# Kernel optimization log

Hardware: AMD Instinct MI355X
Metric: run time of the kernel (lower is better)

The kernel has to match this reference:

```python
import jax, jax.numpy as jnp
import numpy as np

B, V = 256, 128000
NOISE_MIN = 1e-10


def setup_inputs() -> dict:
    key = jax.random.key(0)
    k_log, k_temp, k_noise = jax.random.split(key, 3)
    logits = jax.random.normal(k_log, (B, V), dtype=jnp.float32)
    temperatures = jax.random.uniform(k_temp, (B,), dtype=jnp.float32)
    # first quarter of rows use greedy decoding (temperature <= 0)
    temperatures = temperatures.at[: B // 4].set(0.0)
    # torch's empty_like().exponential_(1) -> Exp(1) noise, passed explicitly for determinism
    noise = jax.random.exponential(k_noise, (B, V), dtype=jnp.float32)
    return {"logits": logits, "temperatures": temperatures, "noise": noise}


def reference(logits, temperatures, noise):
    logits = logits.astype(jnp.float32)  # [B, V]
    greedy = temperatures <= 0           # [B]
    # avoid div-by-zero on greedy rows; their result is overwritten by jnp.where below
    safe_t = jnp.where(greedy, 1.0, temperatures)
    probs = jax.nn.softmax(logits / safe_t[:, None], axis=-1)          # [B, V]
    sampled_tok = jnp.argmax(probs / jnp.maximum(noise, NOISE_MIN), axis=-1)  # Gumbel-style sampling
    greedy_tok = jnp.argmax(logits, axis=-1)
    return jnp.where(greedy, greedy_tok, sampled_tok).astype(jnp.int64)
```

## Files before the change

kernel.cpp:

```cpp
#include <hip/hip_runtime.h>
#include <math.h>

#define B 256
#define V 128000
#define VVEC (V / 4)
#define NOISE_MIN 1e-10f
#define BLOCK 1024

__device__ __forceinline__ void upd(float v, int i, float& bv, int& bi) {
    if (v > bv || (v == bv && i < bi)) { bv = v; bi = i; }
}

__global__ __launch_bounds__(BLOCK) void sampler_kernel(
    const float* __restrict__ logits,
    const float* __restrict__ temps,
    const float* __restrict__ noise,
    int* __restrict__ out)
{
    const int row = blockIdx.x;
    const float t = temps[row];
    const bool greedy = (t <= 0.0f);
    const float invT = greedy ? 1.0f : (1.0f / t);

    const size_t base = (size_t)row * V;
    const float4* __restrict__ lg = reinterpret_cast<const float4*>(logits + base);
    const float4* __restrict__ nz = reinterpret_cast<const float4*>(noise + base);

    float bestVal = -INFINITY;
    int   bestIdx = 0x7FFFFFFF;

    if (greedy) {
        for (int v = threadIdx.x; v < VVEC; v += BLOCK) {
            float4 l = lg[v];
            int i0 = v << 2;
            upd(l.x, i0 + 0, bestVal, bestIdx);
            upd(l.y, i0 + 1, bestVal, bestIdx);
            upd(l.z, i0 + 2, bestVal, bestIdx);
            upd(l.w, i0 + 3, bestVal, bestIdx);
        }
    } else {
        for (int v = threadIdx.x; v < VVEC; v += BLOCK) {
            float4 l = lg[v];
            float4 n = nz[v];
            int i0 = v << 2;
            float kx = l.x * invT - __logf(fmaxf(n.x, NOISE_MIN));
            float ky = l.y * invT - __logf(fmaxf(n.y, NOISE_MIN));
            float kz = l.z * invT - __logf(fmaxf(n.z, NOISE_MIN));
            float kw = l.w * invT - __logf(fmaxf(n.w, NOISE_MIN));
            upd(kx, i0 + 0, bestVal, bestIdx);
            upd(ky, i0 + 1, bestVal, bestIdx);
            upd(kz, i0 + 2, bestVal, bestIdx);
            upd(kw, i0 + 3, bestVal, bestIdx);
        }
    }

    #pragma unroll
    for (int off = 32; off > 0; off >>= 1) {
        float ov = __shfl_down(bestVal, off, 64);
        int   oi = __shfl_down(bestIdx, off, 64);
        if (ov > bestVal || (ov == bestVal && oi < bestIdx)) { bestVal = ov; bestIdx = oi; }
    }

    __shared__ float sVal[BLOCK / 64];
    __shared__ int   sIdx[BLOCK / 64];
    const int wave = threadIdx.x >> 6;
    const int lane = threadIdx.x & 63;
    if (lane == 0) { sVal[wave] = bestVal; sIdx[wave] = bestIdx; }
    __syncthreads();

    if (wave == 0) {
        const int nw = BLOCK / 64;
        bestVal = (lane < nw) ? sVal[lane] : -INFINITY;
        bestIdx = (lane < nw) ? sIdx[lane] : 0x7FFFFFFF;
        #pragma unroll
        for (int off = 8; off > 0; off >>= 1) {
            float ov = __shfl_down(bestVal, off, 64);
            int   oi = __shfl_down(bestIdx, off, 64);
            if (ov > bestVal || (ov == bestVal && oi < bestIdx)) { bestVal = ov; bestIdx = oi; }
        }
        if (lane == 0) out[row] = bestIdx;
    }
}

extern "C" void kernel_launch(void* const* d_in, const int* in_sizes, int n_in,
                              void* d_out, int out_size, void* d_ws, size_t ws_size,
                              hipStream_t stream) {
    const float* logits = (const float*)d_in[0];
    const float* temps  = (const float*)d_in[1];
    const float* noise  = (const float*)d_in[2];
    int* out = (int*)d_out;

    sampler_kernel<<<B, BLOCK, 0, stream>>>(logits, temps, noise, out);
}
```

Before: 267.6 us.

## Split each row across segment blocks and merge argmax with packed 64-bit atomicMax

Each row is now processed by 8 blocks of 256 threads instead of one 1024-thread block, giving 2048 blocks to spread across the GPU instead of 256. Value and index are packed into an order-preserving 64-bit key, so the wave reduction uses one 64-bit shuffle and compare per step. Per-wave results are merged with a global atomicMax into a zeroed workspace. A memset and a small decode kernel are added, which adds launch overhead and atomic contention in exchange for better occupancy.

```diff
diff --git a/kernel.cpp b/kernel.cpp
--- a/kernel.cpp
+++ b/kernel.cpp
@@ -3,9 +3,20 @@
 
 #define B 256
 #define V 128000
-#define VVEC (V / 4)
+#define S 8
+#define SEGV (V / S / 4)
+#define BLOCK 256
 #define NOISE_MIN 1e-10f
-#define BLOCK 1024
+
+__device__ __forceinline__ unsigned int enc_f32(float f) {
+    unsigned int b = __float_as_uint(f);
+    return (b & 0x80000000u) ? ~b : (b | 0x80000000u);
+}
+
+__device__ __forceinline__ unsigned long long pack(float v, int i) {
+    return ((unsigned long long)enc_f32(v) << 32) |
+           (unsigned int)(0x7FFFFFFF - i);
+}
 
 __device__ __forceinline__ void upd(float v, int i, float& bv, int& bi) {
     if (v > bv || (v == bv && i < bi)) { bv = v; bi = i; }
@@ -15,9 +26,10 @@
     const float* __restrict__ logits,
     const float* __restrict__ temps,
     const float* __restrict__ noise,
-    int* __restrict__ out)
+    unsigned long long* __restrict__ ws)
 {
-    const int row = blockIdx.x;
+    const int seg = blockIdx.x;
+    const int row = blockIdx.y;
     const float t = temps[row];
     const bool greedy = (t <= 0.0f);
     const float invT = greedy ? 1.0f : (1.0f / t);
@@ -26,11 +38,14 @@
     const float4* __restrict__ lg = reinterpret_cast<const float4*>(logits + base);
     const float4* __restrict__ nz = reinterpret_cast<const float4*>(noise + base);
 
+    const int start = seg * SEGV;
+    const int end   = start + SEGV;
+
     float bestVal = -INFINITY;
     int   bestIdx = 0x7FFFFFFF;
 
     if (greedy) {
-        for (int v = threadIdx.x; v < VVEC; v += BLOCK) {
+        for (int v = start + threadIdx.x; v < end; v += BLOCK) {
             float4 l = lg[v];
             int i0 = v << 2;
             upd(l.x, i0 + 0, bestVal, bestIdx);
@@ -39,7 +54,7 @@
             upd(l.w, i0 + 3, bestVal, bestIdx);
         }
     } else {
-        for (int v = threadIdx.x; v < VVEC; v += BLOCK) {
+        for (int v = start + threadIdx.x; v < end; v += BLOCK) {
             float4 l = lg[v];
             float4 n = nz[v];
             int i0 = v << 2;
@@ -54,32 +69,24 @@
         }
     }
 
+    unsigned long long best = pack(bestVal, bestIdx);
     #pragma unroll
     for (int off = 32; off > 0; off >>= 1) {
-        float ov = __shfl_down(bestVal, off, 64);
-        int   oi = __shfl_down(bestIdx, off, 64);
-        if (ov > bestVal || (ov == bestVal && oi < bestIdx)) { bestVal = ov; bestIdx = oi; }
+        unsigned long long o = __shfl_down(best, off, 64);
+        if (o > best) best = o;
     }
 
-    __shared__ float sVal[BLOCK / 64];
-    __shared__ int   sIdx[BLOCK / 64];
-    const int wave = threadIdx.x >> 6;
     const int lane = threadIdx.x & 63;
-    if (lane == 0) { sVal[wave] = bestVal; sIdx[wave] = bestIdx; }
-    __syncthreads();
+    if (lane == 0) {
+        atomicMax(&ws[row], best);
+    }
+}
 
-    if (wave == 0) {
-        const int nw = BLOCK / 64;
-        bestVal = (lane < nw) ? sVal[lane] : -INFINITY;
-        bestIdx = (lane < nw) ? sIdx[lane] : 0x7FFFFFFF;
-        #pragma unroll
-        for (int off = 8; off > 0; off >>= 1) {
-            float ov = __shfl_down(bestVal, off, 64);
-            int   oi = __shfl_down(bestIdx, off, 64);
-            if (ov > bestVal || (ov == bestVal && oi < bestIdx)) { bestVal = ov; bestIdx = oi; }
-        }
-        if (lane == 0) out[row] = bestIdx;
-    }
+__global__ void decode_kernel(const unsigned long long* __restrict__ ws,
+                              int* __restrict__ out)
+{
+    int i = threadIdx.x;
+    out[i] = 0x7FFFFFFF - (int)(ws[i] & 0xFFFFFFFFu);
 }
 
 extern "C" void kernel_launch(void* const* d_in, const int* in_sizes, int n_in,
@@ -89,6 +96,11 @@
     const float* temps  = (const float*)d_in[1];
     const float* noise  = (const float*)d_in[2];
     int* out = (int*)d_out;
+    unsigned long long* ws = (unsigned long long*)d_ws;
 
-    sampler_kernel<<<B, BLOCK, 0, stream>>>(logits, temps, noise, out);
+    hipMemsetAsync(ws, 0, B * sizeof(unsigned long long), stream);
+
+    dim3 grid(S, B);
+    sampler_kernel<<<grid, BLOCK, 0, stream>>>(logits, temps, noise, ws);
+    decode_kernel<<<1, B, 0, stream>>>(ws, out);
 }
```

Result: slower. 273.3 us (+2.1%).
